# Kernel optimization log

Hardware: AMD Instinct MI355X
Metric: run time of the kernel (lower is better)

The kernel has to match this reference:

```python
import jax, jax.numpy as jnp
import numpy as np

K_HOPS = 3
ALPHA = 0.3
DELTA = 0.5
KL_EPS = 1e-10
BN_EPS = 1e-5
DEG_MIN = 1e-6

B, T, N, F_IN, H, T_OUT = 8, 12, 1536, 1, 64, 12
HID2 = 2 * H  # MLP hidden width = 128


def setup_inputs() -> dict:
    key = jax.random.key(0)
    ks = jax.random.split(key, 20)
    s = 0.05
    TH = T * H
    inp = {
        "x": jax.random.normal(ks[0], (B, T, N, F_IN), jnp.float32),
        # AdaptiveBiDiffConv weights (stored as (in, out))
        "W1": jax.random.normal(ks[1], (F_IN, H), jnp.float32) * s,
        "W2": jax.random.normal(ks[2], (F_IN, H), jnp.float32) * s,
        # encoder MLPBlock: Linear(TH,128) ReLU Linear(128,128) ReLU Linear(128,64) + proj(TH,64), BN(64)
        "enc_w1": jax.random.normal(ks[3], (TH, HID2), jnp.float32) * s,
        "enc_b1": jnp.zeros((HID2,), jnp.float32),
        "enc_w2": jax.random.normal(ks[4], (HID2, HID2), jnp.float32) * s,
        "enc_b2": jnp.zeros((HID2,), jnp.float32),
        "enc_w3": jax.random.normal(ks[5], (HID2, H), jnp.float32) * s,
        "enc_b3": jnp.zeros((H,), jnp.float32),
        "enc_proj": jax.random.normal(ks[6], (TH, H), jnp.float32) * s,
        "enc_bn_g": jnp.ones((H,), jnp.float32),
        "enc_bn_b": jnp.zeros((H,), jnp.float32),
        "enc_bn_m": jnp.zeros((H,), jnp.float32),
        "enc_bn_v": jnp.ones((H,), jnp.float32),
        # decoder MLPBlock: Linear(64,128) ReLU Linear(128,128) ReLU Linear(128,12) + proj(64,12), BN(12)
        "dec_w1": jax.random.normal(ks[7], (H, HID2), jnp.float32) * s,
        "dec_b1": jnp.zeros((HID2,), jnp.float32),
        "dec_w2": jax.random.normal(ks[8], (HID2, HID2), jnp.float32) * s,
        "dec_b2": jnp.zeros((HID2,), jnp.float32),
        "dec_w3": jax.random.normal(ks[9], (HID2, T_OUT), jnp.float32) * s,
        "dec_b3": jnp.zeros((T_OUT,), jnp.float32),
        "dec_proj": jax.random.normal(ks[10], (H, T_OUT), jnp.float32) * s,
        "dec_bn_g": jnp.ones((T_OUT,), jnp.float32),
        "dec_bn_b": jnp.zeros((T_OUT,), jnp.float32),
        "dec_bn_m": jnp.zeros((T_OUT,), jnp.float32),
        "dec_bn_v": jnp.ones((T_OUT,), jnp.float32),
    }
    return inp


def _row_norm(A):
    return A / jnp.maximum(A.sum(-1, keepdims=True), DEG_MIN)


def _mlp_block(z, w1, b1, w2, b2, w3, b3, proj, g, be, m, v):
    h = jax.nn.relu(z @ w1 + b1)
    h = jax.nn.relu(h @ w2 + b2)
    o = (h @ w3 + b3) + z @ proj
    # BatchNorm1d, eval mode over last (channel) axis
    return (o - m) / jnp.sqrt(v + BN_EPS) * g + be


def _forward(x, W1, W2,
             enc_w1, enc_b1, enc_w2, enc_b2, enc_w3, enc_b3, enc_proj,
             enc_bn_g, enc_bn_b, enc_bn_m, enc_bn_v,
             dec_w1, dec_b1, dec_w2, dec_b2, dec_w3, dec_b3, dec_proj,
             dec_bn_g, dec_bn_b, dec_bn_m, dec_bn_v):
    b, t, n, _ = x.shape
    # ---- KL adjacency (fused form: avoids (B,N,N,T) broadcast) ----
    p = jax.nn.softmax(jnp.transpose(x[..., 0], (0, 2, 1)), axis=-1)  # (B,N,T)
    logp = jnp.log(p + KL_EPS)
    # kl[b,i,j] = sum_t p_i (logp_i - logp_j)
    kl = jnp.sum(p * logp, axis=-1, keepdims=True) - jnp.einsum('bit,bjt->bij', p, logp)
    A = (kl < DELTA).astype(x.dtype)  # (B,N,N)
    A_fwd = _row_norm(A)
    A_bwd = _row_norm(jnp.swapaxes(A, -1, -2))
    # ---- bidirectional diffusion conv (x_k never updated in original loop) ----
    x_flow = x[..., :1]                    # (B,T,N,1)
    x_res = x_flow @ W1                    # (B,T,N,H)
    xw = x_flow @ W2                       # (B,T,N,H)
    fwd = jnp.einsum('bij,btjh->btih', A_fwd, xw)
    bwd = jnp.einsum('bij,btjh->btih', A_bwd, xw)
    x_p = jax.nn.relu(x_res + K_HOPS * (ALPHA * fwd + (1.0 - ALPHA) * bwd))
    # ---- temporal MLP encoder/decoder ----
    x_flat = jnp.transpose(x_p, (0, 2, 1, 3)).reshape(b, n, t * x_p.shape[-1])  # (B,N,T*H)
    x_e = _mlp_block(x_flat, enc_w1, enc_b1, enc_w2, enc_b2, enc_w3, enc_b3,
                     enc_proj, enc_bn_g, enc_bn_b, enc_bn_m, enc_bn_v)  # (B,N,H)
    x_d = _mlp_block(x_e, dec_w1, dec_b1, dec_w2, dec_b2, dec_w3, dec_b3,
                     dec_proj, dec_bn_g, dec_bn_b, dec_bn_m, dec_bn_v)  # (B,N,T_out)
    return jnp.transpose(x_d, (0, 2, 1))[..., None]  # (B,T_out,N,1)


def reference(x, W1, W2,
              enc_w1, enc_b1, enc_w2, enc_b2, enc_w3, enc_b3, enc_proj,
              enc_bn_g, enc_bn_b, enc_bn_m, enc_bn_v,
              dec_w1, dec_b1, dec_w2, dec_b2, dec_w3, dec_b3, dec_proj,
              dec_bn_g, dec_bn_b, dec_bn_m, dec_bn_v):
    return _forward(x, W1, W2,
                    enc_w1, enc_b1, enc_w2, enc_b2, enc_w3, enc_b3, enc_proj,
                    enc_bn_g, enc_bn_b, enc_bn_m, enc_bn_v,
                    dec_w1, dec_b1, dec_w2, dec_b2, dec_w3, dec_b3, dec_proj,
                    dec_bn_g, dec_bn_b, dec_bn_m, dec_bn_v)
```

## Files before the change

### kernel.cpp

```cpp
#include <hip/hip_runtime.h>
#include <hip/hip_bf16.h>


namespace {

constexpr int Bn = 8, Nn = 1536, TOUT = 12;
constexpr int Mrows = Bn * Nn;
constexpr int JS = 8;

typedef __attribute__((ext_vector_type(8))) short bf8;
typedef __attribute__((ext_vector_type(4))) float f4;
typedef unsigned short ush;

__device__ __forceinline__ float b2f(__hip_bfloat16 v) { return __bfloat162float(v); }
__device__ __forceinline__ ush f2bu(float f) {
  union { __hip_bfloat16 h; ush u; } c; c.h = __float2bfloat16(f); return c.u;
}
__device__ __forceinline__ float bu2f(ush u) {
  union { unsigned int i; float f; } c; c.i = ((unsigned)u) << 16; return c.f;
}
__device__ __forceinline__ float ldraw(const void* p, size_t i, int fl) {
  return fl ? ((const float*)p)[i] : b2f(((const __hip_bfloat16*)p)[i]);
}

__device__ __forceinline__ int detect_fl(const void* x, int tid) {
  __shared__ int cnt;
  if (tid == 0) cnt = 0;
  __syncthreads();
  const ush* u = (const ush*)x;
  int c = 0;
#pragma unroll
  for (int s = 0; s < 16; ++s) {
    ush v = u[tid + s * 256];
    if (((v >> 7) & 0xFF) >= 140) c++;
  }
  atomicAdd(&cnt, c);
  __syncthreads();
  return (cnt > 64) ? 1 : 0;
}

struct SmallTab { const void* src[16]; int n[16]; int off[16]; };
struct RepTab { const void* src[8]; int Nc[8]; int NCT[8]; int lb[9]; };

__global__ __launch_bounds__(256) void prep_all(
    const void* __restrict__ xraw, SmallTab st, RepTab rt,
    int* __restrict__ flag, float* __restrict__ CS,
    float* __restrict__ xT, float* __restrict__ sd,
    ush* __restrict__ pA, ush* __restrict__ lA,
    ush* __restrict__ phi16, ush* __restrict__ plo16,
    ush* __restrict__ lhi16, ush* __restrict__ llo16,
    ush* __restrict__ Xc, ush* __restrict__ Wf) {
  int tid = threadIdx.x;
  int fl = detect_fl(xraw, tid);
  int blk = blockIdx.x;

  if (blk < 48) {
    int row = blk * 256 + tid;
    int b = row / Nn, n = row - b * Nn;
    float xv[12];
#pragma unroll
    for (int t = 0; t < 12; ++t)
      xv[t] = ldraw(xraw, (size_t)(b * 12 + t) * Nn + n, fl);
    float mx = xv[0];
#pragma unroll
    for (int t = 1; t < 12; ++t) mx = fmaxf(mx, xv[t]);
    float e[12], Z = 0.f;
#pragma unroll
    for (int t = 0; t < 12; ++t) { e[t] = expf(xv[t] - mx); Z += e[t]; }
    float invZ = 1.f / Z;
    float sacc = 0.f;
    ush pa[32], la[32], ph[16], pl[16], lh[16], ll[16];
#pragma unroll
    for (int k = 0; k < 32; ++k) { pa[k] = 0; la[k] = 0; }
#pragma unroll
    for (int k = 0; k < 16; ++k) { ph[k] = 0; pl[k] = 0; lh[k] = 0; ll[k] = 0; }
#pragma unroll
    for (int t = 0; t < 12; ++t) {
      float pv = e[t] * invZ;
      float lv = logf(pv + 1e-10f);
      sacc += pv * lv;
      xT[(size_t)row * 12 + t] = xv[t];
      ush phv = f2bu(pv);  float plv = pv - bu2f(phv);
      ush lhv = f2bu(lv);  float llv = lv - bu2f(lhv);
      pa[t] = phv; pa[16 + t] = f2bu(plv);
      la[t] = lhv; la[16 + t] = f2bu(llv);
      ph[t] = phv; pl[t] = f2bu(plv);
      lh[t] = lhv; ll[t] = f2bu(llv);
      Xc[((size_t)(b * 16 + t)) * Nn + n] = f2bu(xv[t]);
    }
    Xc[((size_t)(b * 16 + 12)) * Nn + n] = 0x3F80;
#pragma unroll
    for (int t = 13; t < 16; ++t) Xc[((size_t)(b * 16 + t)) * Nn + n] = 0;
    sd[row] = sacc;
    {
      uint4* d = (uint4*)(pA + (size_t)row * 32);
      const uint4* s = (const uint4*)pa;
      d[0] = s[0]; d[1] = s[1]; d[2] = s[2]; d[3] = s[3];
      uint4* d2 = (uint4*)(lA + (size_t)row * 32);
      const uint4* s2 = (const uint4*)la;
      d2[0] = s2[0]; d2[1] = s2[1]; d2[2] = s2[2]; d2[3] = s2[3];
      ((uint4*)(phi16 + (size_t)row * 16))[0] = ((const uint4*)ph)[0];
      ((uint4*)(phi16 + (size_t)row * 16))[1] = ((const uint4*)ph)[1];
      ((uint4*)(plo16 + (size_t)row * 16))[0] = ((const uint4*)pl)[0];
      ((uint4*)(plo16 + (size_t)row * 16))[1] = ((const uint4*)pl)[1];
      ((uint4*)(lhi16 + (size_t)row * 16))[0] = ((const uint4*)lh)[0];
      ((uint4*)(lhi16 + (size_t)row * 16))[1] = ((const uint4*)lh)[1];
      ((uint4*)(llo16 + (size_t)row * 16))[0] = ((const uint4*)ll)[0];
      ((uint4*)(llo16 + (size_t)row * 16))[1] = ((const uint4*)ll)[1];
    }
  } else if (blk < 146) {
    int idx = (blk - 48) * 256 + tid;
    if (idx >= rt.lb[8]) return;
    int mi = 0;
#pragma unroll
    for (int i = 1; i < 8; ++i) if (idx >= rt.lb[i]) mi = i;
    int li = idx - rt.lb[mi];
    int NCT = rt.NCT[mi], Nc = rt.Nc[mi];
    int per = NCT * 64;
    int c0 = li / per, rem = li - c0 * per;
    int ct = rem >> 6, l = rem & 63;
    int q = l >> 4, m = l & 15;
    int col = ct * 16 + m;
    ush* d = Wf + (size_t)idx * 8;
#pragma unroll
    for (int j = 0; j < 8; ++j) {
      int k = c0 * 32 + q * 8 + j;
      d[j] = (col < Nc) ? f2bu(ldraw(rt.src[mi], (size_t)k * Nc + col, fl)) : 0;
    }
  } else {
    for (int i = 0; i < 16; ++i)
      for (int e = tid; e < st.n[i]; e += 256)
        CS[st.off[i] + e] = ldraw(st.src[i], e, fl);
    if (tid == 0) flag[0] = fl;
  }
}

__global__ __launch_bounds__(256) void kl_mfma(
    const ush* __restrict__ pA, const ush* __restrict__ lA,
    const ush* __restrict__ phi16, const ush* __restrict__ plo16,
    const ush* __restrict__ lhi16, const ush* __restrict__ llo16,
    const ush* __restrict__ Xc, const float* __restrict__ sd,
    float* __restrict__ psf, float* __restrict__ psb) {
  __shared__ ush T1[4][512], T2[4][512];
  int tid = threadIdx.x, w = tid >> 6, l = tid & 63, q = l >> 4, n = l & 15;
  int blk = blockIdx.x;
  int b = blk / 192, rem = blk % 192, ig = rem >> 3, js = rem & 7;
  int i0 = ig * 64 + w * 16;
  int rowb = b * Nn;

  if (q >= 2) {
    uint4 z4 = {0, 0, 0, 0};
    *(uint4*)(&T1[w][(size_t)l * 8]) = z4;
    *(uint4*)(&T2[w][(size_t)l * 8]) = z4;
  }

  bf8 z8 = {0, 0, 0, 0, 0, 0, 0, 0};
  bf8 aP = *(const bf8*)(pA + ((size_t)(rowb + i0 + n)) * 32 + q * 8);
  bf8 aL = *(const bf8*)(lA + ((size_t)(rowb + i0 + n)) * 32 + q * 8);
  bf8 aPh = (q < 2) ? aP : z8;
  bf8 aLh = (q < 2) ? aL : z8;
  float selfI[4];
#pragma unroll
  for (int r = 0; r < 4; ++r) selfI[r] = sd[rowb + i0 + q * 4 + r];

  f4 accF = {0.f, 0.f, 0.f, 0.f}, accB = {0.f, 0.f, 0.f, 0.f};

  for (int jt = 0; jt < 12; ++jt) {
    int jl = js * 192 + jt * 16;
    size_t bb = ((size_t)(rowb + jl + n)) * 16 + (q & 1) * 8;
    bf8 bLh = *(const bf8*)(lhi16 + bb);
    bf8 bLo = *(const bf8*)(llo16 + bb);
    bf8 bPh = *(const bf8*)(phi16 + bb);
    bf8 bPo = *(const bf8*)(plo16 + bb);
    float selfJ = sd[rowb + jl + n];

    f4 s1 = {0.f, 0.f, 0.f, 0.f}, s2 = {0.f, 0.f, 0.f, 0.f};
    s1 = __builtin_amdgcn_mfma_f32_16x16x32_bf16(aP, bLh, s1, 0, 0, 0);
    s1 = __builtin_amdgcn_mfma_f32_16x16x32_bf16(aPh, bLo, s1, 0, 0, 0);
    s2 = __builtin_amdgcn_mfma_f32_16x16x32_bf16(aL, bPh, s2, 0, 0, 0);
    s2 = __builtin_amdgcn_mfma_f32_16x16x32_bf16(aLh, bPo, s2, 0, 0, 0);

    int qk = n >> 3, kj = n & 7;
#pragma unroll
    for (int r = 0; r < 4; ++r) {
      int pos = (qk * 16 + q * 4 + r) * 8 + kj;
      T1[w][pos] = (selfI[r] - s1[r] < 0.5f) ? (ush)0x3F80 : (ush)0;
      T2[w][pos] = (selfJ - s2[r] < 0.5f) ? (ush)0x3F80 : (ush)0;
    }
    bf8 af1 = *(const bf8*)(&T1[w][(size_t)l * 8]);
    bf8 af2 = *(const bf8*)(&T2[w][(size_t)l * 8]);
    bf8 xfr = (q < 2)
        ? *(const bf8*)(Xc + ((size_t)(b * 16 + n)) * Nn + jl + q * 8) : z8;
    accF = __builtin_amdgcn_mfma_f32_16x16x32_bf16(af1, xfr, accF, 0, 0, 0);
    accB = __builtin_amdgcn_mfma_f32_16x16x32_bf16(af2, xfr, accB, 0, 0, 0);
  }
#pragma unroll
  for (int r = 0; r < 4; ++r) {
    size_t o = ((size_t)js * Mrows + rowb + i0 + q * 4 + r) * 16 + n;
    psf[o] = accF[r];
    psb[o] = accB[r];
  }
}

__global__ __launch_bounds__(256) void fused_mlp(
    const float* __restrict__ xT,
    const float* __restrict__ psf, const float* __restrict__ psb,
    const float* __restrict__ CS, const ush* __restrict__ Wf,
    const int* __restrict__ flag, void* __restrict__ outp) {
  __shared__ float xs[16][12], ccs[16][12];
  __shared__ float sfs[16][16], sbs[16][16];
  __shared__ float ws1[64], ws2[64];
  __shared__ ush hf[2048], hg[2048], xf[1024];
  __shared__ f4 red[4][64];

  int tid = threadIdx.x, w = tid >> 6, l = tid & 63, q = l >> 4, n = l & 15;
  int r0 = blockIdx.x * 16;

  {
    int r = tid >> 4, t = tid & 15;
    float a = 0.f, b = 0.f;
#pragma unroll
    for (int js = 0; js < JS; ++js) {
      size_t o = ((size_t)js * Mrows + r0 + r) * 16 + t;
      a += psf[o];
      b += psb[o];
    }
    sfs[r][t] = a;
    sbs[r][t] = b;
    if (tid < 128) { if (tid < 64) ws1[tid] = CS[tid]; else ws2[tid - 64] = CS[tid]; }
    if (tid < 192) {
      int rr = tid / 12, tt = tid - rr * 12;
      xs[rr][tt] = xT[(size_t)(r0 + rr) * 12 + tt];
    }
  }
  __syncthreads();
  if (tid < 192) {
    int rr = tid / 12, tt = tid - rr * 12;
    float irs = 1.f / fmaxf(sfs[rr][12], 1e-6f);
    float ics = 1.f / fmaxf(sbs[rr][12], 1e-6f);
    ccs[rr][tt] = 3.0f * (0.3f * sfs[rr][tt] * irs + 0.7f * sbs[rr][tt] * ics);
  }
  __syncthreads();

  auto zregen = [&](int c0) -> bf8 {
    int t = c0 >> 1, h0 = (c0 & 1) * 32 + q * 8;
    float xv = xs[n][t], cv = ccs[n][t];
    union { bf8 v; ush u[8]; } au;
#pragma unroll
    for (int j = 0; j < 8; ++j)
      au.u[j] = f2bu(fmaxf(fmaf(xv, ws1[h0 + j], cv * ws2[h0 + j]), 0.f));
    return au.v;
  };
  auto fpos = [&](int ct, int r) -> int {
    return ((ct >> 1) * 64 + ((ct & 1) * 2 + (n >> 3)) * 16 + q * 4 + r) * 8 + (n & 7);
  };

  {
    f4 a0 = {0.f, 0.f, 0.f, 0.f}, a1 = {0.f, 0.f, 0.f, 0.f};
    for (int c0 = 0; c0 < 24; ++c0) {
      bf8 a = zregen(c0);
      const ush* wb = Wf + ((size_t)(c0 * 8 + 2 * w) * 64 + l) * 8;
      bf8 b0 = *(const bf8*)wb;
      bf8 b1 = *(const bf8*)(wb + 512);
      a0 = __builtin_amdgcn_mfma_f32_16x16x32_bf16(a, b0, a0, 0, 0, 0);
      a1 = __builtin_amdgcn_mfma_f32_16x16x32_bf16(a, b1, a1, 0, 0, 0);
    }
#pragma unroll
    for (int u2 = 0; u2 < 2; ++u2) {
      int ct = 2 * w + u2;
      f4 acc = u2 ? a1 : a0;
      float bz = CS[128 + ct * 16 + n];
#pragma unroll
      for (int r = 0; r < 4; ++r)
        hf[fpos(ct, r)] = f2bu(fmaxf(acc[r] + bz, 0.f));
    }
  }
  __syncthreads();

  {
    f4 a0 = {0.f, 0.f, 0.f, 0.f}, a1 = {0.f, 0.f, 0.f, 0.f};
    for (int c0 = 0; c0 < 4; ++c0) {
      bf8 a = *(const bf8*)(&hf[(size_t)(c0 * 64 + l) * 8]);
      const ush* wb = Wf + 98304 + ((size_t)(c0 * 8 + 2 * w) * 64 + l) * 8;
      bf8 b0 = *(const bf8*)wb;
      bf8 b1 = *(const bf8*)(wb + 512);
      a0 = __builtin_amdgcn_mfma_f32_16x16x32_bf16(a, b0, a0, 0, 0, 0);
      a1 = __builtin_amdgcn_mfma_f32_16x16x32_bf16(a, b1, a1, 0, 0, 0);
    }
    __syncthreads();
#pragma unroll
    for (int u2 = 0; u2 < 2; ++u2) {
      int ct = 2 * w + u2;
      f4 acc = u2 ? a1 : a0;
      float bz = CS[256 + ct * 16 + n];
#pragma unroll
      for (int r = 0; r < 4; ++r)
        hg[fpos(ct, r)] = f2bu(fmaxf(acc[r] + bz, 0.f));
    }
  }
  __syncthreads();

  {
    f4 a3 = {0.f, 0.f, 0.f, 0.f};
    for (int c0 = 0; c0 < 4; ++c0) {
      bf8 a = *(const bf8*)(&hg[(size_t)(c0 * 64 + l) * 8]);
      bf8 b = *(const bf8*)(Wf + 114688 + ((size_t)(c0 * 4 + w) * 64 + l) * 8);
      a3 = __builtin_amdgcn_mfma_f32_16x16x32_bf16(a, b, a3, 0, 0, 0);
    }
    for (int c0 = 0; c0 < 24; ++c0) {
      bf8 a = zregen(c0);
      bf8 b = *(const bf8*)(Wf + 122880 + ((size_t)(c0 * 4 + w) * 64 + l) * 8);
      a3 = __builtin_amdgcn_mfma_f32_16x16x32_bf16(a, b, a3, 0, 0, 0);
    }
    int col = w * 16 + n;
    float g = CS[448 + col], be = CS[512 + col], mm = CS[576 + col], vv = CS[640 + col];
    float sc = g / sqrtf(vv + 1e-5f);
    float sh = be - mm * sc;
    float bz = CS[384 + col];
#pragma unroll
    for (int r = 0; r < 4; ++r)
      xf[fpos(w, r)] = f2bu((a3[r] + bz) * sc + sh);
  }
  __syncthreads();

  {
    f4 a0 = {0.f, 0.f, 0.f, 0.f}, a1 = {0.f, 0.f, 0.f, 0.f};
    for (int c0 = 0; c0 < 2; ++c0) {
      bf8 a = *(const bf8*)(&xf[(size_t)(c0 * 64 + l) * 8]);
      const ush* wb = Wf + 172032 + ((size_t)(c0 * 8 + 2 * w) * 64 + l) * 8;
      bf8 b0 = *(const bf8*)wb;
      bf8 b1 = *(const bf8*)(wb + 512);
      a0 = __builtin_amdgcn_mfma_f32_16x16x32_bf16(a, b0, a0, 0, 0, 0);
      a1 = __builtin_amdgcn_mfma_f32_16x16x32_bf16(a, b1, a1, 0, 0, 0);
    }
    __syncthreads();
#pragma unroll
    for (int u2 = 0; u2 < 2; ++u2) {
      int ct = 2 * w + u2;
      f4 acc = u2 ? a1 : a0;
      float bz = CS[704 + ct * 16 + n];
#pragma unroll
      for (int r = 0; r < 4; ++r)
        hf[fpos(ct, r)] = f2bu(fmaxf(acc[r] + bz, 0.f));
    }
  }
  __syncthreads();

  {
    f4 a0 = {0.f, 0.f, 0.f, 0.f}, a1 = {0.f, 0.f, 0.f, 0.f};
    for (int c0 = 0; c0 < 4; ++c0) {
      bf8 a = *(const bf8*)(&hf[(size_t)(c0 * 64 + l) * 8]);
      const ush* wb = Wf + 180224 + ((size_t)(c0 * 8 + 2 * w) * 64 + l) * 8;
      bf8 b0 = *(const bf8*)wb;
      bf8 b1 = *(const bf8*)(wb + 512);
      a0 = __builtin_amdgcn_mfma_f32_16x16x32_bf16(a, b0, a0, 0, 0, 0);
      a1 = __builtin_amdgcn_mfma_f32_16x16x32_bf16(a, b1, a1, 0, 0, 0);
    }
    __syncthreads();
#pragma unroll
    for (int u2 = 0; u2 < 2; ++u2) {
      int ct = 2 * w + u2;
      f4 acc = u2 ? a1 : a0;
      float bz = CS[832 + ct * 16 + n];
#pragma unroll
      for (int r = 0; r < 4; ++r)
        hg[fpos(ct, r)] = f2bu(fmaxf(acc[r] + bz, 0.f));
    }
  }
  __syncthreads();

  {
    f4 ao = {0.f, 0.f, 0.f, 0.f};
    {
      bf8 a = *(const bf8*)(&hg[(size_t)(w * 64 + l) * 8]);
      bf8 b = *(const bf8*)(Wf + 196608 + ((size_t)w * 64 + l) * 8);
      ao = __builtin_amdgcn_mfma_f32_16x16x32_bf16(a, b, ao, 0, 0, 0);
    }
    if (w < 2) {
      bf8 a = *(const bf8*)(&xf[(size_t)(w * 64 + l) * 8]);
      bf8 b = *(const bf8*)(Wf + 198656 + ((size_t)w * 64 + l) * 8);
      ao = __builtin_amdgcn_mfma_f32_16x16x32_bf16(a, b, ao, 0, 0, 0);
    }
    red[w][l] = ao;
  }
  __syncthreads();
  if (w == 0) {
    f4 s = red[0][l] + red[1][l] + red[2][l] + red[3][l];
    int fl = flag[0];
    if (n < 12) {
      float bz = CS[960 + n];
      float g = CS[972 + n], be = CS[984 + n], mm = CS[996 + n], vv = CS[1008 + n];
      float sc = g / sqrtf(vv + 1e-5f);
      float sh = be - mm * sc;
#pragma unroll
      for (int r = 0; r < 4; ++r) {
        int row = r0 + q * 4 + r;
        int bb = row / Nn, nn = row - bb * Nn;
        size_t oi = ((size_t)bb * TOUT + n) * Nn + nn;
        float ov = (s[r] + bz) * sc + sh;
        if (fl) ((float*)outp)[oi] = ov;
        else    ((ush*)outp)[oi] = f2bu(ov);
      }
    }
  }
}

}

extern "C" void kernel_launch(void* const* d_in, const int* in_sizes, int n_in,
                              void* d_out, int out_size, void* d_ws, size_t ws_size,
                              hipStream_t stream) {
  float* f = (float*)d_ws;
  int* flag = (int*)d_ws;
  float* CS  = f + 16;
  float* xT  = f + 1040;
  float* sd  = f + 148496;
  float* psf = f + 160784;
  float* psb = f + 1733648;
  ush* U = (ush*)(f + 3306512);
  ush* pA    = U;
  ush* lA    = U + 393216;
  ush* phi16 = U + 786432;
  ush* plo16 = U + 983040;
  ush* lhi16 = U + 1179648;
  ush* llo16 = U + 1376256;
  ush* Xc    = U + 1572864;
  ush* Wf    = U + 1769472;

  SmallTab st;
  {
    const int idxs[16] = {1, 2, 4, 6, 8, 10, 11, 12, 13, 15, 17, 19, 21, 22, 23, 24};
    const int ns[16]   = {64, 64, 128, 128, 64, 64, 64, 64, 64, 128, 128, 12, 12, 12, 12, 12};
    int off = 0;
    for (int i = 0; i < 16; ++i) {
      st.src[i] = d_in[idxs[i]]; st.n[i] = ns[i]; st.off[i] = off; off += ns[i];
    }
  }
  RepTab rt;
  {
    const int idxs[8]  = {3, 5, 7, 9, 14, 16, 18, 20};
    const int rNc[8]   = {128, 128, 64, 64, 128, 128, 12, 12};
    const int rNCT[8]  = {8, 8, 4, 4, 8, 8, 1, 1};
    const int rlb[9]   = {0, 12288, 14336, 15360, 21504, 22528, 24576, 24832, 24960};
    for (int i = 0; i < 8; ++i) {
      rt.src[i] = d_in[idxs[i]]; rt.Nc[i] = rNc[i]; rt.NCT[i] = rNCT[i];
    }
    for (int i = 0; i < 9; ++i) rt.lb[i] = rlb[i];
  }

  prep_all<<<147, 256, 0, stream>>>(d_in[0], st, rt, flag, CS, xT, sd,
                                    pA, lA, phi16, plo16, lhi16, llo16, Xc, Wf);
  kl_mfma<<<1536, 256, 0, stream>>>(pA, lA, phi16, plo16, lhi16, llo16,
                                    Xc, sd, psf, psb);
  fused_mlp<<<768, 256, 0, stream>>>(xT, psf, psb, CS, Wf, flag, d_out);
}
```

Baseline: 152.5 us.

## Pack two neighbor tiles per aggregation MFMA and cache encoder input in LDS

In the KL graph kernel, two 16-wide neighbor tiles are now thresholded into the shared fragment before each aggregation MFMA. This uses the full K=32 of the MFMA, so the number of aggregation MFMAs and the zero-padding writes are halved. In the fused MLP, the ReLU-projected input fragments are computed once per block into a 24 KB LDS buffer and reused in both the first layer and the projection path. Previously every wave recomputed them in both places. The extra shared memory may lower occupancy of the MLP kernel.

```diff
diff --git a/kernel.cpp b/kernel.cpp
--- a/kernel.cpp
+++ b/kernel.cpp
@@ -148,12 +148,6 @@
   int i0 = ig * 64 + w * 16;
   int rowb = b * Nn;
 
-  if (q >= 2) {
-    uint4 z4 = {0, 0, 0, 0};
-    *(uint4*)(&T1[w][(size_t)l * 8]) = z4;
-    *(uint4*)(&T2[w][(size_t)l * 8]) = z4;
-  }
-
   bf8 z8 = {0, 0, 0, 0, 0, 0, 0, 0};
   bf8 aP = *(const bf8*)(pA + ((size_t)(rowb + i0 + n)) * 32 + q * 8);
   bf8 aL = *(const bf8*)(lA + ((size_t)(rowb + i0 + n)) * 32 + q * 8);
@@ -165,32 +159,35 @@
 
   f4 accF = {0.f, 0.f, 0.f, 0.f}, accB = {0.f, 0.f, 0.f, 0.f};
 
-  for (int jt = 0; jt < 12; ++jt) {
-    int jl = js * 192 + jt * 16;
-    size_t bb = ((size_t)(rowb + jl + n)) * 16 + (q & 1) * 8;
-    bf8 bLh = *(const bf8*)(lhi16 + bb);
-    bf8 bLo = *(const bf8*)(llo16 + bb);
-    bf8 bPh = *(const bf8*)(phi16 + bb);
-    bf8 bPo = *(const bf8*)(plo16 + bb);
-    float selfJ = sd[rowb + jl + n];
-
-    f4 s1 = {0.f, 0.f, 0.f, 0.f}, s2 = {0.f, 0.f, 0.f, 0.f};
-    s1 = __builtin_amdgcn_mfma_f32_16x16x32_bf16(aP, bLh, s1, 0, 0, 0);
-    s1 = __builtin_amdgcn_mfma_f32_16x16x32_bf16(aPh, bLo, s1, 0, 0, 0);
-    s2 = __builtin_amdgcn_mfma_f32_16x16x32_bf16(aL, bPh, s2, 0, 0, 0);
-    s2 = __builtin_amdgcn_mfma_f32_16x16x32_bf16(aLh, bPo, s2, 0, 0, 0);
-
-    int qk = n >> 3, kj = n & 7;
-#pragma unroll
-    for (int r = 0; r < 4; ++r) {
-      int pos = (qk * 16 + q * 4 + r) * 8 + kj;
-      T1[w][pos] = (selfI[r] - s1[r] < 0.5f) ? (ush)0x3F80 : (ush)0;
-      T2[w][pos] = (selfJ - s2[r] < 0.5f) ? (ush)0x3F80 : (ush)0;
+  for (int jp = 0; jp < 6; ++jp) {
+    int jl = js * 192 + jp * 32;
+#pragma unroll
+    for (int hh = 0; hh < 2; ++hh) {
+      int jh = jl + hh * 16;
+      size_t bb = ((size_t)(rowb + jh + n)) * 16 + (q & 1) * 8;
+      bf8 bLh = *(const bf8*)(lhi16 + bb);
+      bf8 bLo = *(const bf8*)(llo16 + bb);
+      bf8 bPh = *(const bf8*)(phi16 + bb);
+      bf8 bPo = *(const bf8*)(plo16 + bb);
+      float selfJ = sd[rowb + jh + n];
+
+      f4 s1 = {0.f, 0.f, 0.f, 0.f}, s2 = {0.f, 0.f, 0.f, 0.f};
+      s1 = __builtin_amdgcn_mfma_f32_16x16x32_bf16(aP, bLh, s1, 0, 0, 0);
+      s1 = __builtin_amdgcn_mfma_f32_16x16x32_bf16(aPh, bLo, s1, 0, 0, 0);
+      s2 = __builtin_amdgcn_mfma_f32_16x16x32_bf16(aL, bPh, s2, 0, 0, 0);
+      s2 = __builtin_amdgcn_mfma_f32_16x16x32_bf16(aLh, bPo, s2, 0, 0, 0);
+
+      int qk = n >> 3, kj = n & 7;
+#pragma unroll
+      for (int r = 0; r < 4; ++r) {
+        int pos = hh * 256 + (qk * 16 + q * 4 + r) * 8 + kj;
+        T1[w][pos] = (selfI[r] - s1[r] < 0.5f) ? (ush)0x3F80 : (ush)0;
+        T2[w][pos] = (selfJ - s2[r] < 0.5f) ? (ush)0x3F80 : (ush)0;
+      }
     }
     bf8 af1 = *(const bf8*)(&T1[w][(size_t)l * 8]);
     bf8 af2 = *(const bf8*)(&T2[w][(size_t)l * 8]);
-    bf8 xfr = (q < 2)
-        ? *(const bf8*)(Xc + ((size_t)(b * 16 + n)) * Nn + jl + q * 8) : z8;
+    bf8 xfr = *(const bf8*)(Xc + ((size_t)(b * 16 + n)) * Nn + jl + q * 8);
     accF = __builtin_amdgcn_mfma_f32_16x16x32_bf16(af1, xfr, accF, 0, 0, 0);
     accB = __builtin_amdgcn_mfma_f32_16x16x32_bf16(af2, xfr, accB, 0, 0, 0);
   }
@@ -211,6 +208,7 @@
   __shared__ float sfs[16][16], sbs[16][16];
   __shared__ float ws1[64], ws2[64];
   __shared__ ush hf[2048], hg[2048], xf[1024];
+  __shared__ ush zf[12288];
   __shared__ f4 red[4][64];
 
   int tid = threadIdx.x, w = tid >> 6, l = tid & 63, q = l >> 4, n = l & 15;
@@ -255,10 +253,18 @@
     return ((ct >> 1) * 64 + ((ct & 1) * 2 + (n >> 3)) * 16 + q * 4 + r) * 8 + (n & 7);
   };
 
+#pragma unroll
+  for (int u = 0; u < 6; ++u) {
+    int c0 = w * 6 + u;
+    bf8 v = zregen(c0);
+    *(bf8*)(&zf[((size_t)c0 * 64 + l) * 8]) = v;
+  }
+  __syncthreads();
+
   {
     f4 a0 = {0.f, 0.f, 0.f, 0.f}, a1 = {0.f, 0.f, 0.f, 0.f};
     for (int c0 = 0; c0 < 24; ++c0) {
-      bf8 a = zregen(c0);
+      bf8 a = *(const bf8*)(&zf[((size_t)c0 * 64 + l) * 8]);
       const ush* wb = Wf + ((size_t)(c0 * 8 + 2 * w) * 64 + l) * 8;
       bf8 b0 = *(const bf8*)wb;
       bf8 b1 = *(const bf8*)(wb + 512);
@@ -308,7 +314,7 @@
       a3 = __builtin_amdgcn_mfma_f32_16x16x32_bf16(a, b, a3, 0, 0, 0);
     }
     for (int c0 = 0; c0 < 24; ++c0) {
-      bf8 a = zregen(c0);
+      bf8 a = *(const bf8*)(&zf[((size_t)c0 * 64 + l) * 8]);
       bf8 b = *(const bf8*)(Wf + 122880 + ((size_t)(c0 * 4 + w) * 64 + l) * 8);
       a3 = __builtin_amdgcn_mfma_f32_16x16x32_bf16(a, b, a3, 0, 0, 0);
     }
```

Measured after the change: 148.9 us. 2.4% less time.
